# Kernel tuning notes

Hardware: AMD Instinct MI355X
Metric: run time of the kernel (lower is better)

## Reference

```python
import jax, jax.numpy as jnp
import numpy as np

NOPE, ROPE, VDIM, QKD = 128, 64, 128, 192
H = 16
EPS = 1e-6
SCALING = QKD ** -0.5


def rms_norm(x, w):
    xf = x.astype(jnp.float32)
    var = jnp.mean(xf * xf, axis=-1, keepdims=True)
    return (w * (xf * jax.lax.rsqrt(var + EPS))).astype(x.dtype)


def rotate_half(x):
    d = x.shape[-1] // 2
    return jnp.concatenate((-x[..., d:], x[..., :d]), axis=-1)


def apply_rope(q, k, cos, sin):
    # cos/sin: [B,S,D] -> unsqueeze head dim
    cos = cos[:, None, :, :]
    sin = sin[:, None, :, :]
    return q * cos + rotate_half(q) * sin, k * cos + rotate_half(k) * sin


def setup_inputs() -> dict:
    key = jax.random.key(0)
    ks = jax.random.split(key, 8)
    B, S, D = 2, 2048, 2048
    pos = jnp.arange(S, dtype=jnp.float32)
    inv_freq = 1.0 / (10000.0 ** (jnp.arange(0, ROPE, 2, dtype=jnp.float32) / ROPE))
    ang = pos[:, None] * inv_freq[None, :]            # [S, ROPE/2]
    emb = jnp.concatenate([ang, ang], axis=-1)        # [S, ROPE]
    cos = jnp.broadcast_to(jnp.cos(emb)[None], (B, S, ROPE))
    sin = jnp.broadcast_to(jnp.sin(emb)[None], (B, S, ROPE))
    s = lambda k, shp, fan: jax.random.normal(k, shp, jnp.float32) * (fan ** -0.5)
    return {
        "hidden_states": jax.random.normal(ks[0], (B, S, D), jnp.float32),
        "cos": cos,
        "sin": sin,
        "q_a_W": s(ks[1], (1536, D), D),
        "q_a_norm_w": jnp.ones((1536,), jnp.float32),
        "q_b_W": s(ks[2], (H * QKD, 1536), 1536),
        "kv_a_W": s(ks[3], (512 + ROPE, D), D),
        "kv_a_norm_w": jnp.ones((512,), jnp.float32),
        "kv_b_W": s(ks[4], (H * (NOPE + VDIM), 512), 512),
        "o_W": s(ks[5], (D, H * VDIM), H * VDIM),
    }


def reference(hidden_states, cos, sin, q_a_W, q_a_norm_w, q_b_W, kv_a_W,
              kv_a_norm_w, kv_b_W, o_W):
    B, S, D = hidden_states.shape
    # low-rank Q path
    q = rms_norm(hidden_states @ q_a_W.T, q_a_norm_w) @ q_b_W.T   # [B,S,H*QKD]
    q = q.reshape(B, S, H, QKD).transpose(0, 2, 1, 3)             # [B,H,S,QKD]
    q_pass, q_rot = q[..., :NOPE], q[..., NOPE:]
    # compressed KV path
    ckv = hidden_states @ kv_a_W.T                                # [B,S,512+ROPE]
    k_lat, k_rot = ckv[..., :512], ckv[..., 512:]
    kv = rms_norm(k_lat, kv_a_norm_w) @ kv_b_W.T                  # [B,S,H*(NOPE+VDIM)]
    kv = kv.reshape(B, S, H, NOPE + VDIM).transpose(0, 2, 1, 3)   # [B,H,S,*]
    k_pass, v = kv[..., :NOPE], kv[..., NOPE:]
    k_rot = k_rot.reshape(B, 1, S, ROPE)
    q_rot, k_rot = apply_rope(q_rot, k_rot, cos, sin)
    k_rot = jnp.broadcast_to(k_rot, (B, H, S, ROPE))
    query = jnp.concatenate((q_pass, q_rot), axis=-1)             # [B,H,S,QKD]
    key = jnp.concatenate((k_pass, k_rot), axis=-1)
    # eager causal attention
    scores = jnp.einsum('bhsd,bhtd->bhst', query, key) * SCALING
    causal = jnp.tril(jnp.ones((S, S), bool))
    scores = jnp.where(causal, scores, jnp.finfo(scores.dtype).min)
    attn = jax.nn.softmax(scores.astype(jnp.float32), axis=-1).astype(query.dtype)
    out = jnp.einsum('bhst,bhtd->bhsd', attn, v)                  # [B,H,S,VDIM]
    out = out.transpose(0, 2, 1, 3).reshape(B, S, H * VDIM)
    return out @ o_W.T
```

## Files before the change

kernel.cpp:

```cpp
#include <hip/hip_runtime.h>
#include <hip/hip_bf16.h>


typedef __bf16 bf16x8 __attribute__((ext_vector_type(8)));
typedef float floatx4 __attribute__((ext_vector_type(4)));
#define BF16 __hip_bfloat16

static __device__ __forceinline__ BF16 f2b(float x) { return __float2bfloat16(x); }
static __device__ __forceinline__ unsigned short b2u(BF16 x) { return *(unsigned short*)&x; }
static __device__ __forceinline__ float fast_exp2(float x) { return __builtin_amdgcn_exp2f(x); }

template<int CTRL>
static __device__ __forceinline__ float dpp_mov(float x) {
  int xi = __builtin_bit_cast(int, x);
  int yi = __builtin_amdgcn_update_dpp(xi, xi, CTRL, 0xF, 0xF, false);
  return __builtin_bit_cast(float, yi);
}
static __device__ __forceinline__ float row_allmax(float x) {
  x = fmaxf(x, dpp_mov<0xB1>(x));
  x = fmaxf(x, dpp_mov<0x4E>(x));
  x = fmaxf(x, dpp_mov<0x141>(x));
  x = fmaxf(x, dpp_mov<0x140>(x));
  return x;
}
static __device__ __forceinline__ float row_allsum(float x) {
  x += dpp_mov<0xB1>(x);
  x += dpp_mov<0x4E>(x);
  x += dpp_mov<0x141>(x);
  x += dpp_mov<0x140>(x);
  return x;
}

static __device__ __forceinline__ void load_lds16(const BF16* g, BF16* l) {
  __builtin_amdgcn_global_load_lds((__attribute__((address_space(1))) void*)(void*)g,
                                   (__attribute__((address_space(3))) void*)(void*)l,
                                   16, 0, 0);
}

struct CastArgs {
  const float* src[6];
  BF16* dst[6];
  long n[6];
};
__global__ void cast_multi_k(CastArgs a) {
  int r = blockIdx.y;
  long n = a.n[r];
  const float* __restrict__ x = a.src[r];
  BF16* __restrict__ y = a.dst[r];
  for (long i = ((long)blockIdx.x * 256 + threadIdx.x) * 4; i + 3 < n;
       i += (long)gridDim.x * 1024) {
    float4 v = *(const float4*)(x + i);
    y[i+0] = f2b(v.x); y[i+1] = f2b(v.y); y[i+2] = f2b(v.z); y[i+3] = f2b(v.w);
  }
}

template<int OUT_MODE>
static __device__ __forceinline__ void gemm_body(
    const BF16* __restrict__ A, const BF16* __restrict__ B, void* __restrict__ C,
    int M, int N, int K, const float* __restrict__ cosb, const float* __restrict__ sinb,
    BF16* __restrict__ P1, BF16* __restrict__ P2, int bx, int by, BF16* As, BF16* Bs) {
  int tid = threadIdx.x, wave = tid >> 6, lane = tid & 63;
  int wr = wave >> 1, wc = wave & 1, lr = lane & 15, quad = lane >> 4;
  long m0 = (long)by * 256, n0 = (long)bx * 128;

  long asrc[4]; int adst[4];
#pragma unroll
  for (int i = 0; i < 4; i++) {
    int c = wave*64 + lane + 512*i;
    int r = c >> 3, k = c & 7;
    asrc[i] = (m0 + r) * (long)K + ((k ^ (r & 7)) << 3);
    adst[i] = wave*512 + i*4096;
  }
  long bsrc[2]; int bdst[2];
#pragma unroll
  for (int i = 0; i < 2; i++) {
    int c = wave*64 + lane + 512*i;
    int r = c >> 3, k = c & 7;
    long bn = n0 + r; if (bn >= N) bn = N - 1;
    bsrc[i] = bn * (long)K + ((k ^ (r & 7)) << 3);
    bdst[i] = wave*512 + i*4096;
  }

  auto stage = [&](int bi, int kt) {
    long k0 = (long)kt << 6;
    BF16* Ad = As + bi*16384;
    BF16* Bd = Bs + bi*8192;
#pragma unroll
    for (int i = 0; i < 4; i++) load_lds16(A + asrc[i] + k0, Ad + adst[i]);
#pragma unroll
    for (int i = 0; i < 2; i++) load_lds16(B + bsrc[i] + k0, Bd + bdst[i]);
  };

  int aoff[4], boff[4];
#pragma unroll
  for (int i = 0; i < 4; i++) aoff[i] = (wr*64 + i*16 + lr) * 64;
#pragma unroll
  for (int j = 0; j < 4; j++) boff[j] = (wc*64 + j*16 + lr) * 64;
  int x0 = ((quad    ) ^ (lr & 7)) << 3;
  int x1 = ((quad ^ 4) ^ (lr & 7)) << 3;

  floatx4 acc[4][4] = {};
  int NT = K >> 6;

  stage(0, 0);
  stage(1, 1);
  asm volatile("s_waitcnt vmcnt(6)" ::: "memory");
  __builtin_amdgcn_s_barrier();

  int cur = 0;
  for (int t = 0; t < NT; t++) {
    const BF16* Ab = As + cur*16384;
    const BF16* Bb = Bs + cur*8192;
    bf16x8 a0[4], a1[4], b0[4], b1[4];
#pragma unroll
    for (int i = 0; i < 4; i++) {
      a0[i] = *(const bf16x8*)(Ab + aoff[i] + x0);
      a1[i] = *(const bf16x8*)(Ab + aoff[i] + x1);
    }
#pragma unroll
    for (int j = 0; j < 4; j++) {
      b0[j] = *(const bf16x8*)(Bb + boff[j] + x0);
      b1[j] = *(const bf16x8*)(Bb + boff[j] + x1);
    }
    asm volatile("s_waitcnt lgkmcnt(0)" ::: "memory");
    __builtin_amdgcn_s_barrier();
    if (t + 2 < NT) stage(cur, t + 2);
    __builtin_amdgcn_s_setprio(1);
#pragma unroll
    for (int i = 0; i < 4; i++)
#pragma unroll
      for (int j = 0; j < 4; j++)
        acc[i][j] = __builtin_amdgcn_mfma_f32_16x16x32_bf16(a0[i], b0[j], acc[i][j], 0, 0, 0);
#pragma unroll
    for (int i = 0; i < 4; i++)
#pragma unroll
      for (int j = 0; j < 4; j++)
        acc[i][j] = __builtin_amdgcn_mfma_f32_16x16x32_bf16(a1[i], b1[j], acc[i][j], 0, 0, 0);
    __builtin_amdgcn_s_setprio(0);
    if (t + 2 < NT)      { asm volatile("s_waitcnt vmcnt(6)" ::: "memory"); }
    else if (t + 1 < NT) { asm volatile("s_waitcnt vmcnt(0)" ::: "memory"); }
    __builtin_amdgcn_s_barrier();
    __builtin_amdgcn_sched_barrier(0);
    cur ^= 1;
  }

  long n0w = n0 + wc*64;
  const float SCALE_L2E = 0.104117546f;
#pragma unroll
  for (int i = 0; i < 4; i++) {
    long tok = m0 + wr*64 + i*16 + quad*4;
    long bb = tok >> 11, s = tok & 2047;
    if (OUT_MODE == 0) {
#pragma unroll
      for (int r = 0; r < 4; r++) {
        long row = tok + r;
#pragma unroll
        for (int j = 0; j < 4; j++) {
          long col = n0w + j*16 + lr;
          if (col < N) ((float*)C)[row*(long)N + col] = acc[i][j][r];
        }
      }
    } else if (OUT_MODE == 2) {
#pragma unroll
      for (int j = 0; j < 4; j++) {
        long col = n0w + j*16 + lr;
        long h = col >> 8, d = col & 255;
        if (d < 128) {
#pragma unroll
          for (int r = 0; r < 4; r++)
            P1[((bb*16 + h)*2048 + s + r)*192 + d] = f2b(acc[i][j][r]);
        } else {
          ushort4 pk;
          pk.x = b2u(f2b(acc[i][j][0])); pk.y = b2u(f2b(acc[i][j][1]));
          pk.z = b2u(f2b(acc[i][j][2])); pk.w = b2u(f2b(acc[i][j][3]));
          *(ushort4*)(P2 + ((bb*16 + h)*128 + d - 128)*2048 + s) = pk;
        }
      }
    } else {
      bool rope = ((n0w % 192) == 128);
#pragma unroll
      for (int r = 0; r < 4; r++) {
        long row = tok + r;
#pragma unroll
        for (int j = 0; j < 4; j++) {
          long col = n0w + j*16 + lr;
          float x = acc[i][j][r], val;
          if (rope) {
            int id = j*16 + lr;
            float partner = acc[i][j^2][r];
            float rot = (j < 2) ? -partner : partner;
            val = x*cosb[row*64 + id] + rot*sinb[row*64 + id];
          } else {
            val = x;
          }
          long h = col / 192, d = col % 192;
          P1[((bb*16 + h)*2048 + s + r)*192 + d] = f2b(val * SCALE_L2E);
        }
      }
    }
  }
}

__global__ __launch_bounds__(512) void gemm0_k(const BF16* __restrict__ A, const BF16* __restrict__ B,
                                               float* __restrict__ C, int M, int N, int K) {
  __shared__ __align__(16) BF16 As[2*256*64];
  __shared__ __align__(16) BF16 Bs[2*128*64];
  gemm_body<0>(A, B, C, M, N, K, nullptr, nullptr, nullptr, nullptr,
               blockIdx.x, blockIdx.y, As, Bs);
}

__global__ __launch_bounds__(512) void gemm_qkv_k(const BF16* __restrict__ qan, const BF16* __restrict__ Wqb,
                                                  const BF16* __restrict__ kvn, const BF16* __restrict__ Wkvb,
                                                  const float* __restrict__ cosb, const float* __restrict__ sinb,
                                                  BF16* __restrict__ Qt, BF16* __restrict__ Kt,
                                                  BF16* __restrict__ Vt) {
  __shared__ __align__(16) BF16 As[2*256*64];
  __shared__ __align__(16) BF16 Bs[2*128*64];
  int bid = blockIdx.x;
  if (bid < 384) {
    gemm_body<3>(qan, Wqb, nullptr, 4096, 3072, 1536, cosb, sinb, Qt, nullptr,
                 bid % 24, bid / 24, As, Bs);
  } else {
    bid -= 384;
    gemm_body<2>(kvn, Wkvb, nullptr, 4096, 4096, 512, nullptr, nullptr, Kt, Vt,
                 bid % 32, bid / 32, As, Bs);
  }
}

__global__ __launch_bounds__(256) void norms_k(const float* __restrict__ qakv,
                                               const float* __restrict__ qw, const float* __restrict__ kw,
                                               const float* __restrict__ cosb, const float* __restrict__ sinb,
                                               BF16* __restrict__ qan, BF16* __restrict__ kvn,
                                               BF16* __restrict__ Kt) {
  long row = blockIdx.x;
  const float* xr = qakv + row * 2112;
  int tid = threadIdx.x;
  __shared__ float red[4];
  {
    float ss = 0.f;
    for (int i = tid*4; i < 1536; i += 1024) {
      float4 v = *(const float4*)(xr + i);
      ss += v.x*v.x + v.y*v.y + v.z*v.z + v.w*v.w;
    }
#pragma unroll
    for (int off = 32; off > 0; off >>= 1) ss += __shfl_down(ss, off);
    if ((tid & 63) == 0) red[tid >> 6] = ss;
    __syncthreads();
    float rs = rsqrtf((red[0]+red[1]+red[2]+red[3]) / 1536.f + 1e-6f);
    BF16* yr = qan + row * 1536;
    for (int i = tid*4; i < 1536; i += 1024) {
      float4 v = *(const float4*)(xr + i);
      yr[i+0] = f2b(v.x * qw[i+0] * rs);
      yr[i+1] = f2b(v.y * qw[i+1] * rs);
      yr[i+2] = f2b(v.z * qw[i+2] * rs);
      yr[i+3] = f2b(v.w * qw[i+3] * rs);
    }
  }
  __syncthreads();
  {
    float ss = 0.f;
    for (int i = tid*4; i < 512; i += 1024) {
      float4 v = *(const float4*)(xr + 1536 + i);
      ss += v.x*v.x + v.y*v.y + v.z*v.z + v.w*v.w;
    }
#pragma unroll
    for (int off = 32; off > 0; off >>= 1) ss += __shfl_down(ss, off);
    if ((tid & 63) == 0) red[tid >> 6] = ss;
    __syncthreads();
    float rs = rsqrtf((red[0]+red[1]+red[2]+red[3]) / 512.f + 1e-6f);
    BF16* yr = kvn + row * 512;
    for (int i = tid*4; i < 512; i += 1024) {
      float4 v = *(const float4*)(xr + 1536 + i);
      yr[i+0] = f2b(v.x * kw[i+0] * rs);
      yr[i+1] = f2b(v.y * kw[i+1] * rs);
      yr[i+2] = f2b(v.z * kw[i+2] * rs);
      yr[i+3] = f2b(v.w * kw[i+3] * rs);
    }
  }
  if (tid < 64) {
    int i = tid;
    const float* kr = xr + 2048;
    float x = kr[i];
    float rot = (i < 32) ? -kr[i + 32] : kr[i - 32];
    BF16 v = f2b(x * cosb[row*64 + i] + rot * sinb[row*64 + i]);
    long b = row >> 11, s = row & 2047;
    long base = ((b*16)*2048 + s)*192 + 128 + i;
#pragma unroll
    for (int h = 0; h < 16; h++) Kt[base + (long)h*2048*192] = v;
  }
}

#define LK 200
#define LV 72
#define LP 72
__global__ __launch_bounds__(512) void flash_k(const BF16* __restrict__ Qt, const BF16* __restrict__ Kt,
                                               const BF16* __restrict__ Vt, BF16* __restrict__ O) {
  __shared__ __align__(16) BF16 Ks[2][64*LK];
  __shared__ __align__(16) BF16 Vs[2][128*LV];
  __shared__ __align__(16) BF16 Ps[8][16*LP];
  int tid = threadIdx.x, wave = tid >> 6, lane = tid & 63;
  int lr = lane & 15, quad = lane >> 4;
  int F = blockIdx.x;
  int g = F & 31, u = F >> 5;
  int qt = (u < 8) ? u : 23 - u;
  int h = g & 15, b = g >> 4;
  const BF16* Qb = Qt + ((long)(b*16 + h) * 2048) * 192;
  const BF16* Kb = Kt + ((long)(b*16 + h) * 2048) * 192;
  const BF16* Vb = Vt + ((long)(b*16 + h) * 128) * 2048;
  const float NEG_INF = -__builtin_inff();

  int krow[3], kcol[3];
#pragma unroll
  for (int i = 0; i < 3; i++) {
    int c = tid + 512*i;
    krow[i] = c / 24; kcol[i] = (c % 24) * 8;
  }
  int vrow[2], vcol[2];
#pragma unroll
  for (int i = 0; i < 2; i++) {
    int c = tid + 512*i;
    vrow[i] = c >> 3; vcol[i] = (c & 7) * 8;
  }

  bf16x8 kreg[3], vreg[2];
  auto stage_load = [&](int k0) {
#pragma unroll
    for (int i = 0; i < 3; i++)
      kreg[i] = *(const bf16x8*)(Kb + (long)(k0 + krow[i])*192 + kcol[i]);
#pragma unroll
    for (int i = 0; i < 2; i++)
      vreg[i] = *(const bf16x8*)(Vb + (long)vrow[i]*2048 + k0 + vcol[i]);
  };
  auto stage_store = [&](int s) {
#pragma unroll
    for (int i = 0; i < 3; i++)
      *(bf16x8*)(&Ks[s][krow[i]*LK + kcol[i]]) = kreg[i];
#pragma unroll
    for (int i = 0; i < 2; i++)
      *(bf16x8*)(&Vs[s][vrow[i]*LV + vcol[i]]) = vreg[i];
  };

  {
    int q0 = qt * 128;
    int wq0 = q0 + wave*16;
    bf16x8 qf[6];
    {
      const BF16* qp = Qb + (long)(wq0 + lr) * 192 + quad*8;
#pragma unroll
      for (int f = 0; f < 6; f++) qf[f] = *(const bf16x8*)(qp + f*32);
    }
    float m_i[4], l_i[4];
#pragma unroll
    for (int r = 0; r < 4; r++) { m_i[r] = NEG_INF; l_i[r] = 0.f; }
    floatx4 o_acc[8] = {};
    int nk = 2*qt + 2;
    stage_load(0);
    stage_store(0);
    __syncthreads();
    int cur = 0;
    for (int kt = 0; kt < nk; kt++) {
      if (kt + 1 < nk) stage_load((kt + 1) * 64);
      if (kt*64 <= wq0 + 15) {
        const BF16* Kc = Ks[cur];
        const BF16* Vc = Vs[cur];
        floatx4 st[4];
        __builtin_amdgcn_s_setprio(1);
#pragma unroll
        for (int t = 0; t < 4; t++) {
          floatx4 c = {};
#pragma unroll
          for (int f = 0; f < 6; f++) {
            bf16x8 kf = *(const bf16x8*)(Kc + (t*16+lr)*LK + f*32 + quad*8);
            c = __builtin_amdgcn_mfma_f32_16x16x32_bf16(qf[f], kf, c, 0, 0, 0);
          }
          st[t] = c;
        }
        __builtin_amdgcn_s_setprio(0);
        float mt[4];
#pragma unroll
        for (int r = 0; r < 4; r++) mt[r] = NEG_INF;
        if (kt*64 + 63 > wq0) {
          int rbase = wq0 + quad*4 - kt*64;
#pragma unroll
          for (int t = 0; t < 4; t++) {
            int coff = t*16 + lr;
#pragma unroll
            for (int r = 0; r < 4; r++) {
              float sc = st[t][r];
              if (coff > rbase + r) sc = NEG_INF;
              st[t][r] = sc;
              mt[r] = fmaxf(mt[r], sc);
            }
          }
        } else {
#pragma unroll
          for (int t = 0; t < 4; t++)
#pragma unroll
            for (int r = 0; r < 4; r++) mt[r] = fmaxf(mt[r], st[t][r]);
        }
#pragma unroll
        for (int r = 0; r < 4; r++) mt[r] = row_allmax(mt[r]);
        float gr = fmaxf(fmaxf(mt[0]-m_i[0], mt[1]-m_i[1]),
                         fmaxf(mt[2]-m_i[2], mt[3]-m_i[3]));
        gr = fmaxf(gr, __shfl_xor(gr, 16));
        gr = fmaxf(gr, __shfl_xor(gr, 32));
        if (gr > 8.f) {
#pragma unroll
          for (int r = 0; r < 4; r++) {
            float mn = fmaxf(m_i[r], mt[r]);
            float alpha = fast_exp2(m_i[r] - mn);
            m_i[r] = mn;
            l_i[r] *= alpha;
#pragma unroll
            for (int v = 0; v < 8; v++) o_acc[v][r] *= alpha;
          }
        }
        float rsum[4];
#pragma unroll
        for (int r = 0; r < 4; r++) rsum[r] = 0.f;
#pragma unroll
        for (int t = 0; t < 4; t++)
#pragma unroll
          for (int r = 0; r < 4; r++) {
            float p = fast_exp2(st[t][r] - m_i[r]);
            st[t][r] = p;
            rsum[r] += p;
          }
#pragma unroll
        for (int r = 0; r < 4; r++) { rsum[r] = row_allsum(rsum[r]); l_i[r] += rsum[r]; }
#pragma unroll
        for (int t = 0; t < 4; t++)
#pragma unroll
          for (int r = 0; r < 4; r++)
            Ps[wave][(quad*4 + r)*LP + t*16 + lr] = f2b(st[t][r]);
        __builtin_amdgcn_s_setprio(1);
#pragma unroll
        for (int kc = 0; kc < 2; kc++) {
          bf16x8 pa = *(const bf16x8*)(&Ps[wave][lr*LP + kc*32 + quad*8]);
#pragma unroll
          for (int v = 0; v < 8; v++) {
            bf16x8 vf = *(const bf16x8*)(&Vc[(v*16+lr)*LV + kc*32 + quad*8]);
            o_acc[v] = __builtin_amdgcn_mfma_f32_16x16x32_bf16(pa, vf, o_acc[v], 0, 0, 0);
          }
        }
        __builtin_amdgcn_s_setprio(0);
      }
      if (kt + 1 < nk) stage_store(cur ^ 1);
      __syncthreads();
      cur ^= 1;
    }
    long rowb = wq0 + quad*4;
#pragma unroll
    for (int v = 0; v < 8; v++)
#pragma unroll
      for (int r = 0; r < 4; r++) {
        long row = rowb + r;
        O[((long)b*2048 + row)*2048 + h*128 + v*16 + lr] = f2b(o_acc[v][r] / l_i[r]);
      }
  }
}

extern "C" void kernel_launch(void* const* d_in, const int* in_sizes, int n_in,
                              void* d_out, int out_size, void* d_ws, size_t ws_size,
                              hipStream_t stream) {
  const float* hidden      = (const float*)d_in[0];
  const float* cosb        = (const float*)d_in[1];
  const float* sinb        = (const float*)d_in[2];
  const float* q_a_W       = (const float*)d_in[3];
  const float* q_a_norm_w  = (const float*)d_in[4];
  const float* q_b_W       = (const float*)d_in[5];
  const float* kv_a_W      = (const float*)d_in[6];
  const float* kv_a_norm_w = (const float*)d_in[7];
  const float* kv_b_W      = (const float*)d_in[8];
  const float* o_W         = (const float*)d_in[9];
  float* out = (float*)d_out;

  const int Mrows = 4096;

  char* ws = (char*)d_ws; size_t off = 0;
  auto alloc = [&](size_t bytes) -> void* {
    void* p = ws + off; off = (off + bytes + 255) & ~(size_t)255; return p;
  };
  BF16* hb    = (BF16*)alloc((size_t)4096*2048*2);
  BF16* Wqakv = (BF16*)alloc((size_t)2112*2048*2);
  BF16* Wqb   = (BF16*)alloc((size_t)3072*1536*2);
  BF16* Wkvb  = (BF16*)alloc((size_t)4096*512*2);
  BF16* Wo    = (BF16*)alloc((size_t)2048*2048*2);
  float* qakv = (float*)alloc((size_t)4096*2112*4);
  BF16* qan   = (BF16*)alloc((size_t)4096*1536*2);
  BF16* kvn   = (BF16*)alloc((size_t)4096*512*2);
  BF16* Qt    = (BF16*)alloc((size_t)2*16*2048*192*2);
  BF16* Kt    = (BF16*)alloc((size_t)2*16*2048*192*2);
  BF16* Vt    = (BF16*)alloc((size_t)2*16*128*2048*2);
  BF16* attn  = (BF16*)alloc((size_t)4096*2048*2);

  CastArgs ca;
  ca.src[0] = hidden;  ca.dst[0] = hb;                 ca.n[0] = (long)4096*2048;
  ca.src[1] = q_a_W;   ca.dst[1] = Wqakv;              ca.n[1] = (long)1536*2048;
  ca.src[2] = kv_a_W;  ca.dst[2] = Wqakv + (long)1536*2048; ca.n[2] = (long)576*2048;
  ca.src[3] = q_b_W;   ca.dst[3] = Wqb;                ca.n[3] = (long)3072*1536;
  ca.src[4] = kv_b_W;  ca.dst[4] = Wkvb;               ca.n[4] = (long)4096*512;
  ca.src[5] = o_W;     ca.dst[5] = Wo;                 ca.n[5] = (long)2048*2048;
  cast_multi_k<<<dim3(1024, 6), dim3(256), 0, stream>>>(ca);

  gemm0_k<<<dim3(17, 16), dim3(512), 0, stream>>>(hb, Wqakv, qakv, Mrows, 2112, 2048);

  norms_k<<<dim3(4096), dim3(256), 0, stream>>>(qakv, q_a_norm_w, kv_a_norm_w,
                                                cosb, sinb, qan, kvn, Kt);

  gemm_qkv_k<<<dim3(896), dim3(512), 0, stream>>>(qan, Wqb, kvn, Wkvb, cosb, sinb, Qt, Kt, Vt);

  flash_k<<<dim3(512), dim3(512), 0, stream>>>(Qt, Kt, Vt, attn);

  gemm0_k<<<dim3(16, 16), dim3(512), 0, stream>>>(attn, Wo, out, Mrows, 2048, 2048);
}
```

Baseline: 450.1 us.

## Split attention KV tile across wave pairs with 32-row query groups and merge

```diff
diff --git a/kernel.cpp b/kernel.cpp
--- a/kernel.cpp
+++ b/kernel.cpp
@@ -292,14 +292,19 @@
 
 #define LK 200
 #define LV 72
-#define LP 72
+#define LPW 40
 __global__ __launch_bounds__(512) void flash_k(const BF16* __restrict__ Qt, const BF16* __restrict__ Kt,
                                                const BF16* __restrict__ Vt, BF16* __restrict__ O) {
-  __shared__ __align__(16) BF16 Ks[2][64*LK];
-  __shared__ __align__(16) BF16 Vs[2][128*LV];
-  __shared__ __align__(16) BF16 Ps[8][16*LP];
+  __shared__ __align__(16) char smem[108544];
+  BF16* KsB = (BF16*)smem;
+  BF16* VsB = (BF16*)(smem + 51200);
+  BF16* PsB = (BF16*)(smem + 88064);
+  float* Om = (float*)smem;
+  float* Ml = (float*)(smem + 65536);
+
   int tid = threadIdx.x, wave = tid >> 6, lane = tid & 63;
   int lr = lane & 15, quad = lane >> 4;
+  int qg = wave >> 1, kh = wave & 1;
   int F = blockIdx.x;
   int g = F & 31, u = F >> 5;
   int qt = (u < 8) ? u : 23 - u;
@@ -332,130 +337,188 @@
       vreg[i] = *(const bf16x8*)(Vb + (long)vrow[i]*2048 + k0 + vcol[i]);
   };
   auto stage_store = [&](int s) {
+    BF16* Kd = KsB + s*(64*LK);
+    BF16* Vd = VsB + s*(128*LV);
 #pragma unroll
     for (int i = 0; i < 3; i++)
-      *(bf16x8*)(&Ks[s][krow[i]*LK + kcol[i]]) = kreg[i];
+      *(bf16x8*)(Kd + krow[i]*LK + kcol[i]) = kreg[i];
 #pragma unroll
     for (int i = 0; i < 2; i++)
-      *(bf16x8*)(&Vs[s][vrow[i]*LV + vcol[i]]) = vreg[i];
+      *(bf16x8*)(Vd + vrow[i]*LV + vcol[i]) = vreg[i];
   };
 
-  {
-    int q0 = qt * 128;
-    int wq0 = q0 + wave*16;
-    bf16x8 qf[6];
-    {
-      const BF16* qp = Qb + (long)(wq0 + lr) * 192 + quad*8;
-#pragma unroll
-      for (int f = 0; f < 6; f++) qf[f] = *(const bf16x8*)(qp + f*32);
-    }
-    float m_i[4], l_i[4];
-#pragma unroll
-    for (int r = 0; r < 4; r++) { m_i[r] = NEG_INF; l_i[r] = 0.f; }
-    floatx4 o_acc[8] = {};
-    int nk = 2*qt + 2;
-    stage_load(0);
-    stage_store(0);
-    __syncthreads();
-    int cur = 0;
-    for (int kt = 0; kt < nk; kt++) {
-      if (kt + 1 < nk) stage_load((kt + 1) * 64);
-      if (kt*64 <= wq0 + 15) {
-        const BF16* Kc = Ks[cur];
-        const BF16* Vc = Vs[cur];
-        floatx4 st[4];
-        __builtin_amdgcn_s_setprio(1);
-#pragma unroll
-        for (int t = 0; t < 4; t++) {
-          floatx4 c = {};
-#pragma unroll
-          for (int f = 0; f < 6; f++) {
-            bf16x8 kf = *(const bf16x8*)(Kc + (t*16+lr)*LK + f*32 + quad*8);
-            c = __builtin_amdgcn_mfma_f32_16x16x32_bf16(qf[f], kf, c, 0, 0, 0);
-          }
-          st[t] = c;
-        }
-        __builtin_amdgcn_s_setprio(0);
-        float mt[4];
-#pragma unroll
-        for (int r = 0; r < 4; r++) mt[r] = NEG_INF;
-        if (kt*64 + 63 > wq0) {
-          int rbase = wq0 + quad*4 - kt*64;
-#pragma unroll
-          for (int t = 0; t < 4; t++) {
+  int wq0 = qt*128 + qg*32;
+  bf16x8 qf[2][6];
+#pragma unroll
+  for (int s = 0; s < 2; s++) {
+    const BF16* qp = Qb + (long)(wq0 + s*16 + lr) * 192 + quad*8;
+#pragma unroll
+    for (int f = 0; f < 6; f++) qf[s][f] = *(const bf16x8*)(qp + f*32);
+  }
+  float m_i[2][4], l_i[2][4];
+#pragma unroll
+  for (int s = 0; s < 2; s++)
+#pragma unroll
+    for (int r = 0; r < 4; r++) { m_i[s][r] = NEG_INF; l_i[s][r] = 0.f; }
+  floatx4 o_acc[2][8] = {};
+  BF16* Psw = PsB + wave*(32*LPW);
+
+  int nk = 2*qt + 2;
+  stage_load(0);
+  stage_store(0);
+  __syncthreads();
+  int cur = 0;
+  for (int kt = 0; kt < nk; kt++) {
+    if (kt + 1 < nk) stage_load((kt + 1) * 64);
+    int kbase = kt*64 + kh*32;
+    if (kbase <= wq0 + 31) {
+      const BF16* Kc = KsB + cur*(64*LK);
+      const BF16* Vc = VsB + cur*(128*LV);
+      floatx4 st[2][2] = {};
+      __builtin_amdgcn_s_setprio(1);
+#pragma unroll
+      for (int t = 0; t < 2; t++)
+#pragma unroll
+        for (int f = 0; f < 6; f++) {
+          bf16x8 kf = *(const bf16x8*)(Kc + (kh*32 + t*16 + lr)*LK + f*32 + quad*8);
+          st[0][t] = __builtin_amdgcn_mfma_f32_16x16x32_bf16(qf[0][f], kf, st[0][t], 0, 0, 0);
+          st[1][t] = __builtin_amdgcn_mfma_f32_16x16x32_bf16(qf[1][f], kf, st[1][t], 0, 0, 0);
+        }
+      __builtin_amdgcn_s_setprio(0);
+      float mt[2][4];
+#pragma unroll
+      for (int s = 0; s < 2; s++)
+#pragma unroll
+        for (int r = 0; r < 4; r++) mt[s][r] = NEG_INF;
+      if (kbase + 31 > wq0) {
+#pragma unroll
+        for (int s = 0; s < 2; s++) {
+          int rbase = wq0 + s*16 + quad*4 - kbase;
+#pragma unroll
+          for (int t = 0; t < 2; t++) {
             int coff = t*16 + lr;
 #pragma unroll
             for (int r = 0; r < 4; r++) {
-              float sc = st[t][r];
+              float sc = st[s][t][r];
               if (coff > rbase + r) sc = NEG_INF;
-              st[t][r] = sc;
-              mt[r] = fmaxf(mt[r], sc);
+              st[s][t][r] = sc;
+              mt[s][r] = fmaxf(mt[s][r], sc);
             }
           }
-        } else {
-#pragma unroll
-          for (int t = 0; t < 4; t++)
-#pragma unroll
-            for (int r = 0; r < 4; r++) mt[r] = fmaxf(mt[r], st[t][r]);
-        }
-#pragma unroll
-        for (int r = 0; r < 4; r++) mt[r] = row_allmax(mt[r]);
-        float gr = fmaxf(fmaxf(mt[0]-m_i[0], mt[1]-m_i[1]),
-                         fmaxf(mt[2]-m_i[2], mt[3]-m_i[3]));
-        gr = fmaxf(gr, __shfl_xor(gr, 16));
-        gr = fmaxf(gr, __shfl_xor(gr, 32));
-        if (gr > 8.f) {
+        }
+      } else {
+#pragma unroll
+        for (int s = 0; s < 2; s++)
+#pragma unroll
+          for (int t = 0; t < 2; t++)
+#pragma unroll
+            for (int r = 0; r < 4; r++) mt[s][r] = fmaxf(mt[s][r], st[s][t][r]);
+      }
+#pragma unroll
+      for (int s = 0; s < 2; s++)
+#pragma unroll
+        for (int r = 0; r < 4; r++) mt[s][r] = row_allmax(mt[s][r]);
+      float gr = NEG_INF;
+#pragma unroll
+      for (int s = 0; s < 2; s++)
+#pragma unroll
+        for (int r = 0; r < 4; r++) gr = fmaxf(gr, mt[s][r] - m_i[s][r]);
+      gr = fmaxf(gr, __shfl_xor(gr, 16));
+      gr = fmaxf(gr, __shfl_xor(gr, 32));
+      if (gr > 8.f) {
+#pragma unroll
+        for (int s = 0; s < 2; s++)
 #pragma unroll
           for (int r = 0; r < 4; r++) {
-            float mn = fmaxf(m_i[r], mt[r]);
-            float alpha = fast_exp2(m_i[r] - mn);
-            m_i[r] = mn;
-            l_i[r] *= alpha;
-#pragma unroll
-            for (int v = 0; v < 8; v++) o_acc[v][r] *= alpha;
+            float mn = fmaxf(m_i[s][r], mt[s][r]);
+            float alpha = fast_exp2(m_i[s][r] - mn);
+            m_i[s][r] = mn;
+            l_i[s][r] *= alpha;
+#pragma unroll
+            for (int v = 0; v < 8; v++) o_acc[s][v][r] *= alpha;
           }
-        }
-        float rsum[4];
-#pragma unroll
-        for (int r = 0; r < 4; r++) rsum[r] = 0.f;
-#pragma unroll
-        for (int t = 0; t < 4; t++)
+      }
+      float rsum[2][4];
+#pragma unroll
+      for (int s = 0; s < 2; s++)
+#pragma unroll
+        for (int r = 0; r < 4; r++) rsum[s][r] = 0.f;
+#pragma unroll
+      for (int s = 0; s < 2; s++)
+#pragma unroll
+        for (int t = 0; t < 2; t++)
 #pragma unroll
           for (int r = 0; r < 4; r++) {
-            float p = fast_exp2(st[t][r] - m_i[r]);
-            st[t][r] = p;
-            rsum[r] += p;
+            float p = fast_exp2(st[s][t][r] - m_i[s][r]);
+            st[s][t][r] = p;
+            rsum[s][r] += p;
           }
 #pragma unroll
-        for (int r = 0; r < 4; r++) { rsum[r] = row_allsum(rsum[r]); l_i[r] += rsum[r]; }
-#pragma unroll
-        for (int t = 0; t < 4; t++)
+      for (int s = 0; s < 2; s++)
+#pragma unroll
+        for (int r = 0; r < 4; r++) { rsum[s][r] = row_allsum(rsum[s][r]); l_i[s][r] += rsum[s][r]; }
+#pragma unroll
+      for (int s = 0; s < 2; s++)
+#pragma unroll
+        for (int t = 0; t < 2; t++)
 #pragma unroll
           for (int r = 0; r < 4; r++)
-            Ps[wave][(quad*4 + r)*LP + t*16 + lr] = f2b(st[t][r]);
-        __builtin_amdgcn_s_setprio(1);
-#pragma unroll
-        for (int kc = 0; kc < 2; kc++) {
-          bf16x8 pa = *(const bf16x8*)(&Ps[wave][lr*LP + kc*32 + quad*8]);
-#pragma unroll
-          for (int v = 0; v < 8; v++) {
-            bf16x8 vf = *(const bf16x8*)(&Vc[(v*16+lr)*LV + kc*32 + quad*8]);
-            o_acc[v] = __builtin_amdgcn_mfma_f32_16x16x32_bf16(pa, vf, o_acc[v], 0, 0, 0);
-          }
-        }
-        __builtin_amdgcn_s_setprio(0);
-      }
-      if (kt + 1 < nk) stage_store(cur ^ 1);
-      __syncthreads();
-      cur ^= 1;
-    }
-    long rowb = wq0 + quad*4;
-#pragma unroll
-    for (int v = 0; v < 8; v++)
+            Psw[(s*16 + quad*4 + r)*LPW + t*16 + lr] = f2b(st[s][t][r]);
+      bf16x8 pa0 = *(const bf16x8*)(Psw + lr*LPW + quad*8);
+      bf16x8 pa1 = *(const bf16x8*)(Psw + (16 + lr)*LPW + quad*8);
+      __builtin_amdgcn_s_setprio(1);
+#pragma unroll
+      for (int v = 0; v < 8; v++) {
+        bf16x8 vf = *(const bf16x8*)(Vc + (v*16+lr)*LV + kh*32 + quad*8);
+        o_acc[0][v] = __builtin_amdgcn_mfma_f32_16x16x32_bf16(pa0, vf, o_acc[0][v], 0, 0, 0);
+        o_acc[1][v] = __builtin_amdgcn_mfma_f32_16x16x32_bf16(pa1, vf, o_acc[1][v], 0, 0, 0);
+      }
+      __builtin_amdgcn_s_setprio(0);
+    }
+    if (kt + 1 < nk) stage_store(cur ^ 1);
+    __syncthreads();
+    cur ^= 1;
+  }
+
+  if (kh == 1) {
+#pragma unroll
+    for (int s = 0; s < 2; s++)
+#pragma unroll
+      for (int v = 0; v < 8; v++)
+#pragma unroll
+        for (int r = 0; r < 4; r++)
+          Om[(qg*32 + s*16 + quad*4 + r)*128 + v*16 + lr] = o_acc[s][v][r];
+    if (lr == 0) {
+#pragma unroll
+      for (int s = 0; s < 2; s++)
+#pragma unroll
+        for (int r = 0; r < 4; r++) {
+          int row32 = qg*32 + s*16 + quad*4 + r;
+          Ml[row32*2]     = m_i[s][r];
+          Ml[row32*2 + 1] = l_i[s][r];
+        }
+    }
+  }
+  __syncthreads();
+  if (kh == 0) {
+#pragma unroll
+    for (int s = 0; s < 2; s++)
 #pragma unroll
       for (int r = 0; r < 4; r++) {
-        long row = rowb + r;
-        O[((long)b*2048 + row)*2048 + h*128 + v*16 + lr] = f2b(o_acc[v][r] / l_i[r]);
+        int row32 = qg*32 + s*16 + quad*4 + r;
+        float m1 = Ml[row32*2], l1 = Ml[row32*2 + 1];
+        float m0 = m_i[s][r],  l0 = l_i[s][r];
+        float ms = fmaxf(m0, m1);
+        float f0 = fast_exp2(m0 - ms);
+        float f1 = fast_exp2(m1 - ms);
+        float linv = 1.f / (l0*f0 + l1*f1);
+        long rowg = qt*128 + row32;
+#pragma unroll
+        for (int v = 0; v < 8; v++) {
+          float o1 = Om[row32*128 + v*16 + lr];
+          O[((long)b*2048 + rowg)*2048 + h*128 + v*16 + lr] =
+              f2b((o_acc[s][v][r]*f0 + o1*f1) * linv);
+        }
       }
   }
 }
```

New measurement: 457.1 us. No clear change (+1.5%).
